# Kernel optimization log

Hardware: AMD Instinct MI355X
Metric: run time of the kernel (lower is better)

Reference implementation:

```python
import jax, jax.numpy as jnp
import numpy as np

VOCAB = 32000
D_MODEL = 1024
D_FF = 4 * D_MODEL
N_LAYERS = 2
N_EXPERTS = 8
TOP_K = 2
BATCH = 4
SEQ = 2048
LN_EPS = 1e-5


def setup_inputs() -> dict:
    key = jax.random.key(0)
    ks = jax.random.split(key, 12)
    s = lambda *dims: 1.0 / np.sqrt(dims[-2] if len(dims) > 1 else dims[-1])
    inp = {
        "tokens": jax.random.randint(ks[0], (BATCH, SEQ), 0, VOCAB, dtype=jnp.int32),
        "symbolic_emb": jax.random.normal(ks[1], (BATCH, D_MODEL), dtype=jnp.float32),
        "emb": jax.random.normal(ks[2], (VOCAB, D_MODEL), dtype=jnp.float32) * 0.02,
        "gate_w": jax.random.normal(ks[3], (N_LAYERS, D_MODEL, N_EXPERTS), dtype=jnp.float32) / np.sqrt(D_MODEL),
        "gate_b": jnp.zeros((N_LAYERS, N_EXPERTS), dtype=jnp.float32),
        "w1": jax.random.normal(ks[4], (N_LAYERS, N_EXPERTS, D_MODEL, D_FF), dtype=jnp.float32) / np.sqrt(D_MODEL),
        "b1": jnp.zeros((N_LAYERS, N_EXPERTS, D_FF), dtype=jnp.float32),
        "w2": jax.random.normal(ks[5], (N_LAYERS, N_EXPERTS, D_FF, D_MODEL), dtype=jnp.float32) / np.sqrt(D_FF),
        "b2": jnp.zeros((N_LAYERS, N_EXPERTS, D_MODEL), dtype=jnp.float32),
        "ln_g": jnp.ones((D_MODEL,), dtype=jnp.float32),
        "ln_b": jnp.zeros((D_MODEL,), dtype=jnp.float32),
    }
    return inp


def _moe_layer(x_flat, gw, gb, w1, b1, w2, b2):
    # x_flat: [T, d]
    probs = jax.nn.softmax(x_flat @ gw + gb, axis=-1)            # [T, E]
    weights, idx = jax.lax.top_k(probs, TOP_K)                   # [T, K]
    # combine weight per (token, expert): sum of top-k weights routed to that expert
    combine = jnp.sum(jax.nn.one_hot(idx, N_EXPERTS, dtype=x_flat.dtype) * weights[..., None], axis=1)  # [T, E]
    out = jnp.zeros_like(x_flat)
    for j in range(N_EXPERTS):  # small fixed structural loop
        h = jax.nn.gelu(x_flat @ w1[j] + b1[j], approximate=False)  # [T, d_ff]
        y = h @ w2[j] + b2[j]                                       # [T, d]
        out = out + combine[:, j:j + 1] * y
    return out


def reference(tokens, symbolic_emb, emb, gate_w, gate_b, w1, b1, w2, b2, ln_g, ln_b):
    x = emb[tokens] + symbolic_emb[:, None, :]                  # [B, S, d]
    T = BATCH * SEQ
    x = x.reshape(T, D_MODEL)
    for l in range(N_LAYERS):
        x = _moe_layer(x, gate_w[l], gate_b[l], w1[l], b1[l], w2[l], b2[l])
    mu = jnp.mean(x, axis=-1, keepdims=True)
    var = jnp.mean(jnp.square(x - mu), axis=-1, keepdims=True)
    x = (x - mu) * jax.lax.rsqrt(var + LN_EPS) * ln_g + ln_b
    return x.reshape(BATCH, SEQ, D_MODEL)
```

## Files before the change

### kernel.cpp

```cpp
#include <hip/hip_runtime.h>
#include <math.h>

#define T_TOK 8192
#define DM 1024
#define DFF 4096
#define NE 8
#define NPAIR 16384
#define MT256 72
#define MT128 136
#define LN_EPS 1e-5f

typedef __attribute__((ext_vector_type(8))) short bf16x8;
typedef __attribute__((ext_vector_type(4))) float f32x4;
typedef __attribute__((ext_vector_type(4))) unsigned short u16x4;
typedef __attribute__((ext_vector_type(8))) unsigned short u16x8;
typedef unsigned int u32;
typedef unsigned short u16;

__device__ __forceinline__ u16 f2bf(float f) {
  union { float f; u32 u; } v; v.f = f;
  u32 r = (v.u + 0x7fffu + ((v.u >> 16) & 1u)) >> 16;
  return (u16)r;
}
__device__ __forceinline__ float bf2f(u16 h) {
  union { u32 u; float f; } v; v.u = ((u32)h) << 16; return v.f;
}
__device__ __forceinline__ float gelu_exact(float v) {
  return 0.5f * v * (1.0f + erff(v * 0.70710678118654752f));
}
__device__ __forceinline__ float gelu_fast(float v) {
  float u = v * (0.7978845608f + 0.0356774081f * v * v);
  float t = __expf(-2.0f * fabsf(u));
  float th = (1.0f - t) / (1.0f + t);
  th = copysignf(th, u);
  return 0.5f * v * (1.0f + th);
}

__device__ __forceinline__ void gll16(const void* g, void* l) {
  __builtin_amdgcn_global_load_lds(
      (const __attribute__((address_space(1))) u32*)g,
      (__attribute__((address_space(3))) u32*)l, 16, 0, 0);
}

__device__ __forceinline__ void xcd_remap(int& M, int& nt) {
  if (((gridDim.x & 7) == 0) && ((gridDim.y & 7) == 0)) {
    int c = blockIdx.x & 7, q = blockIdx.x >> 3;
    M  = ((blockIdx.y >> 3) << 3) + c;
    nt = (q << 3) + (blockIdx.y & 7);
  } else {
    M = blockIdx.y; nt = blockIdx.x;
  }
}

__global__ __launch_bounds__(256) void embed_gate_kernel(const int* __restrict__ tok,
    const float* __restrict__ sym, const float* __restrict__ emb,
    const float* __restrict__ gw, const float* __restrict__ gb,
    u16* __restrict__ xh, u16* __restrict__ xl,
    int* __restrict__ topk_idx, float* __restrict__ topk_w)
{
  int t = blockIdx.x;
  int b = t >> 11;
  int tk = tok[t];
  int d = threadIdx.x * 4;
  f32x4 e = *(const f32x4*)(emb + (size_t)tk * DM + d);
  f32x4 s = *(const f32x4*)(sym + (size_t)b * DM + d);
  f32x4 v = e + s;
  u16x4 hv, lv;
#pragma unroll
  for (int j = 0; j < 4; ++j) {
    u16 hb = f2bf(v[j]);
    hv[j] = hb;
    lv[j] = f2bf(v[j] - bf2f(hb));
  }
  *(u16x4*)(xh + (size_t)t * DM + d) = hv;
  *(u16x4*)(xl + (size_t)t * DM + d) = lv;

  double a[8] = {0,0,0,0,0,0,0,0};
#pragma unroll
  for (int q = 0; q < 4; ++q) {
    const f32x4* gr = (const f32x4*)(gw + (size_t)(d + q) * 8);
    f32x4 g0 = gr[0], g1 = gr[1];
    double xv = (double)v[q];
    a[0] += xv*(double)g0.x; a[1] += xv*(double)g0.y;
    a[2] += xv*(double)g0.z; a[3] += xv*(double)g0.w;
    a[4] += xv*(double)g1.x; a[5] += xv*(double)g1.y;
    a[6] += xv*(double)g1.z; a[7] += xv*(double)g1.w;
  }
#pragma unroll
  for (int j = 0; j < 8; ++j) {
#pragma unroll
    for (int sh = 32; sh; sh >>= 1) a[j] += __shfl_xor(a[j], sh);
  }
  __shared__ double red[4][8];
  int wave = threadIdx.x >> 6, lane = threadIdx.x & 63;
  if (lane == 0) {
#pragma unroll
    for (int j = 0; j < 8; ++j) red[wave][j] = a[j];
  }
  __syncthreads();
  if (threadIdx.x == 0) {
    double lg[8];
#pragma unroll
    for (int j = 0; j < 8; ++j)
      lg[j] = red[0][j] + red[1][j] + red[2][j] + red[3][j] + (double)gb[j];
    double m = lg[0];
    for (int j = 1; j < 8; ++j) m = lg[j] > m ? lg[j] : m;
    double p[8], sum = 0.0;
    for (int j = 0; j < 8; ++j) { p[j] = exp(lg[j] - m); sum += p[j]; }
    for (int j = 0; j < 8; ++j) p[j] /= sum;
    int j0 = 0; double b0 = p[0];
    for (int j = 1; j < 8; ++j) if (p[j] > b0) { b0 = p[j]; j0 = j; }
    int j1 = (j0 == 0) ? 1 : 0; double b1v = p[j1];
    for (int j = 0; j < 8; ++j) if (j != j0 && p[j] > b1v) { b1v = p[j]; j1 = j; }
    topk_idx[t*2]   = j0; topk_idx[t*2+1] = j1;
    topk_w[t*2]     = (float)b0; topk_w[t*2+1] = (float)b1v;
  }
}

__global__ __launch_bounds__(256) void count_kernel(const int* __restrict__ topk_idx,
    int* __restrict__ meta)
{
  __shared__ int hist[8];
  int tid = threadIdx.x;
  if (tid < 8) hist[tid] = 0;
  __syncthreads();
  int t = blockIdx.x * 256 + tid;
  atomicAdd(&hist[topk_idx[t*2] & 7], 1);
  atomicAdd(&hist[topk_idx[t*2+1] & 7], 1);
  __syncthreads();
  if (tid < 8) meta[256 + blockIdx.x * 8 + tid] = hist[tid];
}

__global__ __launch_bounds__(64) void scan_kernel(int* __restrict__ meta)
{
  __shared__ int tot[8], off[9], tb2[8], tb1[8];
  int lane = threadIdx.x;
  if (lane < 8) {
    int s = 0;
    for (int b = 0; b < 32; ++b) s += meta[256 + b * 8 + lane];
    tot[lane] = s;
  }
  __syncthreads();
  if (lane == 0) {
    int s = 0, n2 = 0, n1 = 0;
    for (int e = 0; e < 8; ++e) {
      off[e] = s; s += tot[e];
      tb2[e] = n2; n2 += (tot[e] + 255) >> 8;
      tb1[e] = n1; n1 += (tot[e] + 127) >> 7;
    }
    off[8] = s;
    for (int i = n2; i < MT256; ++i) meta[32 + i] = -1;
    for (int i = n1; i < MT128; ++i) meta[104 + i] = -1;
  }
  __syncthreads();
  if (lane < 9) meta[8 + lane] = off[lane];
  if (lane < 8) {
    meta[lane] = tot[lane];
    int n2 = (tot[lane] + 255) >> 8;
    for (int i = 0; i < n2; ++i) meta[32 + tb2[lane] + i] = (lane << 16) | i;
    int n1 = (tot[lane] + 127) >> 7;
    for (int i = 0; i < n1; ++i) meta[104 + tb1[lane] + i] = (lane << 16) | i;
    int run = off[lane];
    for (int b = 0; b < 32; ++b) {
      meta[512 + b * 8 + lane] = run;
      run += meta[256 + b * 8 + lane];
    }
  }
}

__global__ __launch_bounds__(256) void scatter_kernel(int* __restrict__ topk_idx,
    const int* __restrict__ meta, int* __restrict__ pair_token)
{
  __shared__ int hist[8];
  __shared__ int base[8];
  int tid = threadIdx.x;
  if (tid < 8) { hist[tid] = 0; base[tid] = meta[512 + blockIdx.x * 8 + tid]; }
  __syncthreads();
  int t = blockIdx.x * 256 + tid;
#pragma unroll
  for (int k = 0; k < 2; ++k) {
    int e = topk_idx[t*2 + k] & 7;
    int pos = atomicAdd(&hist[e], 1);
    int slot = base[e] + pos;
    pair_token[slot] = t;
    topk_idx[t*2 + k] = e | (slot << 3);
  }
}

template<bool LO>
__global__ __launch_bounds__(256) void transpose_kernel(const float* __restrict__ src,
    u16* __restrict__ dsth, u16* __restrict__ dstl, int K, int N)
{
  __shared__ float tile[64][65];
  int e = blockIdx.z;
  const float* s = src + (size_t)e * K * N;
  size_t dbase = (size_t)e * K * N;
  int n0 = blockIdx.x * 64, k0 = blockIdx.y * 64;
  int tid = threadIdx.x;
#pragma unroll
  for (int j = 0; j < 4; ++j) {
    int kl = j * 16 + (tid >> 4);
    int nn = (tid & 15) * 4;
    f32x4 v = *(const f32x4*)(s + (size_t)(k0 + kl) * N + n0 + nn);
    tile[nn + 0][kl] = v.x;
    tile[nn + 1][kl] = v.y;
    tile[nn + 2][kl] = v.z;
    tile[nn + 3][kl] = v.w;
  }
  __syncthreads();
#pragma unroll
  for (int it = 0; it < 2; ++it) {
    int task = it * 256 + tid;
    int nr = task >> 3;
    int ch = task & 7;
    u16x8 oh, ol;
#pragma unroll
    for (int j = 0; j < 8; ++j) {
      float v = tile[nr][ch*8 + j];
      u16 hb = f2bf(v);
      oh[j] = hb;
      if (LO) ol[j] = f2bf(v - bf2f(hb));
    }
    size_t doff = dbase + (size_t)(n0 + nr) * K + k0 + ch*8;
    *(u16x8*)(dsth + doff) = oh;
    if (LO) *(u16x8*)(dstl + doff) = ol;
  }
}

__global__ __launch_bounds__(256) void w2g_kernel(const float* __restrict__ w2,
    const float* __restrict__ gw, float* __restrict__ w2g)
{
  int wid = blockIdx.x * 4 + (threadIdx.x >> 6);
  int lane = threadIdx.x & 63;
  int e = wid >> 12, f = wid & 4095;
  const float* row = w2 + ((size_t)e * DFF + f) * DM;
  float a0=0,a1=0,a2=0,a3=0,a4=0,a5=0,a6=0,a7=0;
  for (int i = 0; i < 4; ++i) {
    int d0 = i * 256 + lane * 4;
    f32x4 xv = *(const f32x4*)(row + d0);
#pragma unroll
    for (int q = 0; q < 4; ++q) {
      const f32x4* gr = (const f32x4*)(gw + (size_t)(d0 + q) * 8);
      f32x4 g0 = gr[0], g1 = gr[1];
      float xq = xv[q];
      a0 += xq*g0.x; a1 += xq*g0.y; a2 += xq*g0.z; a3 += xq*g0.w;
      a4 += xq*g1.x; a5 += xq*g1.y; a6 += xq*g1.z; a7 += xq*g1.w;
    }
  }
  float acc[8] = {a0,a1,a2,a3,a4,a5,a6,a7};
#pragma unroll
  for (int j = 0; j < 8; ++j) {
#pragma unroll
    for (int sh = 32; sh; sh >>= 1) acc[j] += __shfl_xor(acc[j], sh);
  }
  if (lane == 0) {
#pragma unroll
    for (int j = 0; j < 8; ++j) w2g[(size_t)wid * 8 + j] = acc[j];
  }
}

__global__ __launch_bounds__(256) void b2g_kernel(const float* __restrict__ b2,
    const float* __restrict__ gw, float* __restrict__ b2g)
{
  int w = blockIdx.x * 4 + (threadIdx.x >> 6);
  int lane = threadIdx.x & 63;
  int e = w >> 3, j = w & 7;
  float acc = 0.f;
  for (int i = 0; i < 16; ++i) {
    int d = i * 64 + lane;
    acc += b2[(size_t)e * DM + d] * gw[(size_t)d * 8 + j];
  }
#pragma unroll
  for (int sh = 32; sh; sh >>= 1) acc += __shfl_xor(acc, sh);
  if (lane == 0) b2g[w] = acc;
}

__global__ __launch_bounds__(256) void gate1_kernel(const float* __restrict__ Rpart,
    const float* __restrict__ b2g, const float* __restrict__ gb,
    int* __restrict__ topk_idx, float* __restrict__ topk_w)
{
  int t = blockIdx.x * 256 + threadIdx.x;
  int v0 = topk_idx[t*2], v1 = topk_idx[t*2+1];
  int e0 = v0 & 7, e1 = v1 & 7;
  int s0 = v0 >> 3, s1 = v1 >> 3;
  float r0[8] = {0,0,0,0,0,0,0,0}, r1[8] = {0,0,0,0,0,0,0,0};
  for (int nt = 0; nt < 16; ++nt) {
    const float* p0r = Rpart + ((size_t)nt * NPAIR + s0) * 8;
    const float* p1r = Rpart + ((size_t)nt * NPAIR + s1) * 8;
#pragma unroll
    for (int j = 0; j < 8; ++j) { r0[j] += p0r[j]; r1[j] += p1r[j]; }
  }
  double w0 = (double)topk_w[t*2], w1 = (double)topk_w[t*2+1];
  double a[8];
#pragma unroll
  for (int j = 0; j < 8; ++j)
    a[j] = w0 * ((double)r0[j] + (double)b2g[e0*8+j])
         + w1 * ((double)r1[j] + (double)b2g[e1*8+j])
         + (double)gb[j];
  double m = a[0];
  for (int j = 1; j < 8; ++j) m = a[j] > m ? a[j] : m;
  double p[8], sum = 0.0;
  for (int j = 0; j < 8; ++j) { p[j] = exp(a[j] - m); sum += p[j]; }
  for (int j = 0; j < 8; ++j) p[j] /= sum;
  int j0 = 0; double b0 = p[0];
  for (int j = 1; j < 8; ++j) if (p[j] > b0) { b0 = p[j]; j0 = j; }
  int j1 = (j0 == 0) ? 1 : 0; double b1v = p[j1];
  for (int j = 0; j < 8; ++j) if (j != j0 && p[j] > b1v) { b1v = p[j]; j1 = j; }
  topk_idx[t*2]   = j0; topk_idx[t*2+1] = j1;
  topk_w[t*2]     = (float)b0; topk_w[t*2+1] = (float)b1v;
}

template<int K0, int NSEG, int NTOT, bool GATHER>
__global__ __launch_bounds__(512, 2) void gemm256_kernel(
    const u16* __restrict__ Ah, const u16* __restrict__ Al,
    const u16* __restrict__ Bh, const u16* __restrict__ Bl,
    const float* __restrict__ bias, const int* __restrict__ off,
    const int* __restrict__ tiletab, const int* __restrict__ pair_token,
    u16* __restrict__ outh, const float* __restrict__ W2G,
    float* __restrict__ Rpart)
{
  constexpr int NT = (K0 * NSEG) / 64;
  static_assert(NT >= 2 && (NT & 1) == 0, "");
  int Mi, nti;
  xcd_remap(Mi, nti);
  const int tt = tiletab[Mi];
  if (tt < 0) return;
  const int e  = tt >> 16;
  const int mt = tt & 0xffff;
  const int off_e = off[e], off_e1 = off[e + 1];
  const int p0 = off_e + mt * 256;
  const int n0 = nti * 256;

  __shared__ __align__(16) u16 ALs[2][2][8192];
  __shared__ __align__(16) u16 BLs[2][2][8192];

  const int tid  = threadIdx.x;
  const int lane = tid & 63;
  const int wave = tid >> 6;
  const int wm = wave >> 2;
  const int wn = wave & 3;
  const int wbase = tid & 448;

  size_t aoff[2], boff[2];
#pragma unroll
  for (int i = 0; i < 2; ++i) {
    int c = i * 512 + tid;
    int r = c >> 2;
    int cs = (c & 3) ^ ((r >> 1) & 3);
    int idx = p0 + r;
    if (idx >= off_e1) idx = p0;
    int ar = GATHER ? pair_token[idx] : idx;
    aoff[i] = (size_t)ar * K0 + (size_t)(cs * 8);
    boff[i] = ((size_t)e * NTOT + n0 + r) * K0 + (size_t)(cs * 8);
  }

  auto stageA = [&](int t, int kh) {
    int kk = t * 64 + kh * 32;
    int seg = (NSEG == 3) ? (kk >> 10) : 0;
    int kc  = (NSEG == 3) ? (kk & (K0 - 1)) : kk;
    const u16* base = (NSEG == 3 && seg == 1) ? Al : Ah;
    u16* dst = &ALs[t & 1][kh][0];
#pragma unroll
    for (int i = 0; i < 2; ++i)
      gll16(base + aoff[i] + kc, dst + (i * 512 + wbase) * 8);
  };
  auto stageB = [&](int t, int kh) {
    int kk = t * 64 + kh * 32;
    int seg = (NSEG == 3) ? (kk >> 10) : 0;
    int kc  = (NSEG == 3) ? (kk & (K0 - 1)) : kk;
    const u16* base = (NSEG == 3 && seg == 2) ? Bl : Bh;
    u16* dst = &BLs[t & 1][kh][0];
#pragma unroll
    for (int i = 0; i < 2; ++i)
      gll16(base + boff[i] + kc, dst + (i * 512 + wbase) * 8);
  };

  f32x4 acc[8][4];
  const f32x4 fzero = {0.f, 0.f, 0.f, 0.f};
#pragma unroll
  for (int m = 0; m < 8; ++m)
#pragma unroll
    for (int n = 0; n < 4; ++n) acc[m][n] = fzero;

  const int swzB = (((lane >> 4) ^ (((lane & 15) >> 1) & 3)) << 4);
  const char* Abase = (const char*)&ALs[0][0][0]
      + (wm * 128 + (lane & 15)) * 64 + swzB;
  const char* Bbase = (const char*)&BLs[0][0][0]
      + (wn * 64 + (lane & 15)) * 64 + swzB;

#define RDA4(dst, POFS, MB)                                                     \
  { _Pragma("unroll") for (int mf = 0; mf < 4; ++mf)                            \
      dst[mf] = *(const bf16x8*)(Abase + (POFS) + ((MB) + mf) * 1024); }
#define RDB4(dst, POFS)                                                         \
  { _Pragma("unroll") for (int nf = 0; nf < 4; ++nf)                            \
      dst[nf] = *(const bf16x8*)(Bbase + (POFS) + nf * 1024); }

#define MMBLK(MB, A4, B4)                                                       \
  {                                                                             \
    __builtin_amdgcn_s_setprio(1);                                              \
    _Pragma("unroll")                                                           \
    for (int mf = 0; mf < 4; ++mf)                                              \
      _Pragma("unroll")                                                         \
      for (int nf = 0; nf < 4; ++nf)                                            \
        acc[(MB) + mf][nf] = __builtin_amdgcn_mfma_f32_16x16x32_bf16(           \
            (A4)[mf], (B4)[nf], acc[(MB) + mf][nf], 0, 0, 0);                   \
    __builtin_amdgcn_s_setprio(0);                                              \
  }

#define TILE256(t, POFS)                                                        \
  {                                                                             \
    bf16x8 bA[4], aA[4], aB[4], bC[4], aC[4], aD[4];                            \
    RDB4(bA, (POFS));                                                           \
    RDA4(aA, (POFS), 0);                                                        \
    if ((t) + 1 < NT) stageA((t) + 1, 1);                                       \
    __builtin_amdgcn_s_barrier();                                               \
    MMBLK(0, aA, bA);                                                           \
    __builtin_amdgcn_s_barrier();                                               \
    RDA4(aB, (POFS), 4);                                                        \
    if ((t) + 1 < NT) stageB((t) + 1, 1);                                       \
    __builtin_amdgcn_s_barrier();                                               \
    MMBLK(4, aB, bA);                                                           \
    if ((t) + 1 < NT) { asm volatile("s_waitcnt vmcnt(8)" ::: "memory"); }      \
    else              { asm volatile("s_waitcnt vmcnt(0)" ::: "memory"); }      \
    __builtin_amdgcn_s_barrier();                                               \
    asm volatile("" ::: "memory");                                              \
    RDB4(bC, (POFS) + 16384);                                                   \
    RDA4(aC, (POFS) + 16384, 0);                                                \
    if ((t) + 2 < NT) stageA((t) + 2, 0);                                       \
    __builtin_amdgcn_s_barrier();                                               \
    MMBLK(0, aC, bC);                                                           \
    __builtin_amdgcn_s_barrier();                                               \
    RDA4(aD, (POFS) + 16384, 4);                                                \
    if ((t) + 2 < NT) stageB((t) + 2, 0);                                       \
    __builtin_amdgcn_s_barrier();                                               \
    MMBLK(4, aD, bC);                                                           \
    if ((t) + 1 < NT) {                                                         \
      if ((t) + 2 < NT) { asm volatile("s_waitcnt vmcnt(8)" ::: "memory"); }    \
      else              { asm volatile("s_waitcnt vmcnt(4)" ::: "memory"); }    \
      __builtin_amdgcn_s_barrier();                                             \
      asm volatile("" ::: "memory");                                            \
    }                                                                           \
  }

  stageA(0, 0); stageB(0, 0);
  stageA(0, 1); stageB(0, 1);
  stageA(1, 0); stageB(1, 0);
  asm volatile("s_waitcnt vmcnt(8)" ::: "memory");
  __builtin_amdgcn_s_barrier();
  asm volatile("" ::: "memory");

  for (int t = 0; t < NT; t += 2) {
    TILE256(t, 0);
    TILE256(t + 1, 32768);
  }
#undef TILE256
#undef MMBLK
#undef RDA4
#undef RDB4

  float bv[4];
#pragma unroll
  for (int nf = 0; nf < 4; ++nf)
    bv[nf] = bias[(size_t)e * NTOT + n0 + wn * 64 + nf * 16 + (lane & 15)];

  __syncthreads();
  float* Rpt = (float*)&ALs[0][0][0];
  f32x4 wg0[4], wg1[4];
#pragma unroll
  for (int nf = 0; nf < 4; ++nf) {
    int col = n0 + wn * 64 + nf * 16 + (lane & 15);
    const float* wp = W2G + ((size_t)e * NTOT + col) * 8;
    wg0[nf] = *(const f32x4*)wp;
    wg1[nf] = *(const f32x4*)(wp + 4);
  }
#pragma unroll
  for (int mf = 0; mf < 8; ++mf) {
    f32x4 pr0[4], pr1[4];
#pragma unroll
    for (int r = 0; r < 4; ++r) { pr0[r] = fzero; pr1[r] = fzero; }
    int rbase = p0 + wm * 128 + mf * 16 + ((lane >> 4) << 2);
#pragma unroll
    for (int nf = 0; nf < 4; ++nf) {
      int col = n0 + wn * 64 + nf * 16 + (lane & 15);
#pragma unroll
      for (int r = 0; r < 4; ++r) {
        float v = gelu_exact(acc[mf][nf][r] + bv[nf]);
        if (rbase + r < off_e1)
          outh[(size_t)(rbase + r) * NTOT + col] = f2bf(v);
        pr0[r] += v * wg0[nf];
        pr1[r] += v * wg1[nf];
      }
    }
#pragma unroll
    for (int r = 0; r < 4; ++r) {
#pragma unroll
      for (int sh = 1; sh < 16; sh <<= 1) {
#pragma unroll
        for (int q = 0; q < 4; ++q) {
          pr0[r][q] += __shfl_xor(pr0[r][q], sh);
          pr1[r][q] += __shfl_xor(pr1[r][q], sh);
        }
      }
      if ((lane & 15) == 0) {
        int rl = wm * 128 + mf * 16 + ((lane >> 4) << 2) + r;
        float* dst = Rpt + ((size_t)(wn * 256 + rl)) * 8;
        *(f32x4*)dst = pr0[r];
        *(f32x4*)(dst + 4) = pr1[r];
      }
    }
  }
  __syncthreads();
  for (int i = tid; i < 256 * 8; i += 512) {
    int rl = i >> 3, j = i & 7;
    float ssum = Rpt[(size_t)(0 * 256 + rl) * 8 + j]
               + Rpt[(size_t)(1 * 256 + rl) * 8 + j]
               + Rpt[(size_t)(2 * 256 + rl) * 8 + j]
               + Rpt[(size_t)(3 * 256 + rl) * 8 + j];
    int p = p0 + rl;
    if (p < off_e1)
      Rpart[((size_t)nti * NPAIR + p) * 8 + j] = ssum;
  }
}

template<int K0, int NTOT, bool GATHER, int MODE>
__global__ __launch_bounds__(256, 4) void gemm128_kernel(
    const u16* __restrict__ Ah, const u16* __restrict__ Bh,
    const float* __restrict__ bias, const int* __restrict__ off,
    const int* __restrict__ tiletab, const int* __restrict__ pair_token,
    u16* __restrict__ outp)
{
  constexpr int NT = K0 / 32;
  static_assert((NT & 1) == 0, "");
  int Mi, nti;
  xcd_remap(Mi, nti);
  const int tt = tiletab[Mi];
  if (tt < 0) return;
  const int e  = tt >> 16;
  const int mt = tt & 0xffff;
  const int off_e = off[e], off_e1 = off[e + 1];
  const int p0 = off_e + mt * 128;
  const int n0 = nti * 128;

  __shared__ __align__(16) u16 AL[2][4096];
  __shared__ __align__(16) u16 BL[2][4096];

  const int tid  = threadIdx.x;
  const int lane = tid & 63;
  const int wave = tid >> 6;
  const int wm = wave >> 1, wn = wave & 1;
  const int wbase = tid & 192;

  size_t aoff[2], boff[2];
#pragma unroll
  for (int i = 0; i < 2; ++i) {
    int c = i * 256 + tid;
    int r = c >> 2;
    int cs = (c & 3) ^ ((r >> 1) & 3);
    int idx = p0 + r;
    if (idx >= off_e1) idx = p0;
    int ar = GATHER ? pair_token[idx] : idx;
    aoff[i] = (size_t)ar * K0 + (size_t)(cs * 8);
    boff[i] = ((size_t)e * NTOT + n0 + r) * K0 + (size_t)(cs * 8);
  }

  auto stage = [&](int b, int t) {
    int kc = t * 32;
#pragma unroll
    for (int i = 0; i < 2; ++i) {
      int cb = i * 256 + wbase;
      gll16(Ah + aoff[i] + kc, &AL[b][cb * 8]);
      gll16(Bh + boff[i] + kc, &BL[b][cb * 8]);
    }
  };

  f32x4 acc[4][4];
  const f32x4 fzero = {0.f, 0.f, 0.f, 0.f};
#pragma unroll
  for (int m = 0; m < 4; ++m)
#pragma unroll
    for (int n = 0; n < 4; ++n) acc[m][n] = fzero;

  const int swzB = (((lane >> 4) ^ (((lane & 15) >> 1) & 3)) << 4);
  const char* Abase = (const char*)&AL[0][0]
      + (wm * 64 + (lane & 15)) * 64 + swzB;
  const char* Bbase = (const char*)&BL[0][0]
      + (wn * 64 + (lane & 15)) * 64 + swzB;

#define MMA128(BOFS)                                                            \
  {                                                                             \
    bf16x8 af[4], bf[4];                                                        \
    _Pragma("unroll")                                                           \
    for (int m = 0; m < 4; ++m)                                                 \
      af[m] = *(const bf16x8*)(Abase + (BOFS) + m * 1024);                      \
    _Pragma("unroll")                                                           \
    for (int n = 0; n < 4; ++n)                                                 \
      bf[n] = *(const bf16x8*)(Bbase + (BOFS) + n * 1024);                      \
    __builtin_amdgcn_s_setprio(1);                                              \
    _Pragma("unroll")                                                           \
    for (int m = 0; m < 4; ++m)                                                 \
      _Pragma("unroll")                                                         \
      for (int n = 0; n < 4; ++n)                                               \
        acc[m][n] = __builtin_amdgcn_mfma_f32_16x16x32_bf16(                    \
            af[m], bf[n], acc[m][n], 0, 0, 0);                                  \
    __builtin_amdgcn_s_setprio(0);                                              \
  }

  stage(0, 0);
  __syncthreads();

  for (int t = 0; t < NT; t += 2) {
    stage(1, t + 1);
    MMA128(0);
    __syncthreads();
    if (t + 2 < NT) stage(0, t + 2);
    MMA128(8192);
    __syncthreads();
  }
#undef MMA128

  float bv[4];
#pragma unroll
  for (int n = 0; n < 4; ++n)
    bv[n] = bias[(size_t)e * NTOT + n0 + wn * 64 + n * 16 + (lane & 15)];

#pragma unroll
  for (int m = 0; m < 4; ++m) {
    int rbase = p0 + wm * 64 + m * 16 + ((lane >> 4) << 2);
#pragma unroll
    for (int n = 0; n < 4; ++n) {
      int col = n0 + wn * 64 + n * 16 + (lane & 15);
#pragma unroll
      for (int r = 0; r < 4; ++r) {
        int rowp = rbase + r;
        if (rowp < off_e1) {
          float v = acc[m][n][r] + bv[n];
          if constexpr (MODE == 0) v = gelu_fast(v);
          outp[(size_t)rowp * NTOT + col] = f2bf(v);
        }
      }
    }
  }
}

__global__ __launch_bounds__(256) void combine0_kernel(const u16* __restrict__ yb,
    const int* __restrict__ topk_idx, const float* __restrict__ topk_w,
    u16* __restrict__ xh)
{
  int t = blockIdx.x;
  int d = threadIdx.x * 4;
  int s0 = topk_idx[t*2] >> 3, s1 = topk_idx[t*2 + 1] >> 3;
  float w0 = topk_w[t*2], w1 = topk_w[t*2 + 1];
  u16x4 y0 = *(const u16x4*)(yb + (size_t)s0 * DM + d);
  u16x4 y1 = *(const u16x4*)(yb + (size_t)s1 * DM + d);
  u16x4 hv;
#pragma unroll
  for (int j = 0; j < 4; ++j)
    hv[j] = f2bf(bf2f(y0[j]) * w0 + bf2f(y1[j]) * w1);
  *(u16x4*)(xh + (size_t)t * DM + d) = hv;
}

__global__ __launch_bounds__(256) void combine1_ln_kernel(const u16* __restrict__ yb,
    const int* __restrict__ topk_idx, const float* __restrict__ topk_w,
    const float* __restrict__ g, const float* __restrict__ b, float* __restrict__ out)
{
  int t = blockIdx.x;
  int d = threadIdx.x * 4;
  int s0 = topk_idx[t*2] >> 3, s1 = topk_idx[t*2 + 1] >> 3;
  float w0 = topk_w[t*2], w1 = topk_w[t*2 + 1];
  u16x4 y0 = *(const u16x4*)(yb + (size_t)s0 * DM + d);
  u16x4 y1 = *(const u16x4*)(yb + (size_t)s1 * DM + d);
  f32x4 v;
#pragma unroll
  for (int j = 0; j < 4; ++j)
    v[j] = bf2f(y0[j]) * w0 + bf2f(y1[j]) * w1;
  float s = v.x + v.y + v.z + v.w;
  float sq = v.x*v.x + v.y*v.y + v.z*v.z + v.w*v.w;
#pragma unroll
  for (int sh = 32; sh; sh >>= 1) { s += __shfl_xor(s, sh); sq += __shfl_xor(sq, sh); }
  __shared__ float red[8];
  int wave = threadIdx.x >> 6, lane = threadIdx.x & 63;
  if (lane == 0) { red[wave] = s; red[4 + wave] = sq; }
  __syncthreads();
  s = red[0] + red[1] + red[2] + red[3];
  sq = red[4] + red[5] + red[6] + red[7];
  float mu = s * (1.0f / DM);
  float var = sq * (1.0f / DM) - mu * mu;
  float inv = rsqrtf(var + LN_EPS);
  f32x4 gv = *(const f32x4*)(g + d);
  f32x4 bv = *(const f32x4*)(b + d);
  f32x4 o;
  o.x = (v.x - mu) * inv * gv.x + bv.x;
  o.y = (v.y - mu) * inv * gv.y + bv.y;
  o.z = (v.z - mu) * inv * gv.z + bv.z;
  o.w = (v.w - mu) * inv * gv.w + bv.w;
  *(f32x4*)(out + (size_t)t * DM + d) = o;
}

extern "C" void kernel_launch(void* const* d_in, const int* in_sizes, int n_in,
                              void* d_out, int out_size, void* d_ws, size_t ws_size,
                              hipStream_t stream)
{
  const int*   tokens = (const int*)d_in[0];
  const float* sym    = (const float*)d_in[1];
  const float* emb    = (const float*)d_in[2];
  const float* gate_w = (const float*)d_in[3];
  const float* gate_b = (const float*)d_in[4];
  const float* w1     = (const float*)d_in[5];
  const float* b1     = (const float*)d_in[6];
  const float* w2     = (const float*)d_in[7];
  const float* b2     = (const float*)d_in[8];
  const float* ln_g   = (const float*)d_in[9];
  const float* ln_b   = (const float*)d_in[10];

  char* ws = (char*)d_ws;
  u16*   yb  = (u16*)  (ws);
  u16*   xh  = (u16*)  (ws + 33554432);
  u16*   xl  = (u16*)  (ws + 50331648);
  u16*   hh  = (u16*)  (ws + 67108864);
  float* W2G   = (float*)(ws + 201326592);
  float* Rpart = (float*)(ws + 202375168);
  float* B2G   = (float*)(ws + 219152384);
  u16*   wTh = (u16*)  (ws + 335544320);
  u16*   wTl = (u16*)  (ws + 402653184);
  int*   pair_token = (int*)  (ws + 469762048);
  int*   topk_idx   = (int*)  (ws + 469893120);
  float* topk_w     = (float*)(ws + 469958656);
  int*   meta       = (int*)  (ws + 470024192);

  embed_gate_kernel<<<T_TOK, 256, 0, stream>>>(tokens, sym, emb, gate_w, gate_b,
                                               xh, xl, topk_idx, topk_w);
  count_kernel<<<T_TOK / 256, 256, 0, stream>>>(topk_idx, meta);
  scan_kernel<<<1, 64, 0, stream>>>(meta);
  scatter_kernel<<<T_TOK / 256, 256, 0, stream>>>(topk_idx, meta, pair_token);

  w2g_kernel<<<NE * DFF / 4, 256, 0, stream>>>(w2, gate_w + (size_t)DM * NE, W2G);
  b2g_kernel<<<16, 256, 0, stream>>>(b2, gate_w + (size_t)DM * NE, B2G);

  transpose_kernel<true><<<dim3(DFF / 64, DM / 64, NE), 256, 0, stream>>>(
      w1, wTh, wTl, DM, DFF);
  gemm256_kernel<DM, 3, DFF, true><<<dim3(DFF / 256, MT256), 512, 0, stream>>>(
      xh, xl, wTh, wTl, b1, meta + 8, meta + 32, pair_token, hh, W2G, Rpart);

  transpose_kernel<false><<<dim3(DM / 64, DFF / 64, NE), 256, 0, stream>>>(
      w2, wTh, nullptr, DFF, DM);
  gemm128_kernel<DFF, DM, false, 2><<<dim3(DM / 128, MT128), 256, 0, stream>>>(
      hh, wTh, b2, meta + 8, meta + 104, pair_token, yb);

  combine0_kernel<<<T_TOK, 256, 0, stream>>>(yb, topk_idx, topk_w, xh);

  gate1_kernel<<<T_TOK / 256, 256, 0, stream>>>(Rpart, B2G, gate_b + NE,
                                                topk_idx, topk_w);
  count_kernel<<<T_TOK / 256, 256, 0, stream>>>(topk_idx, meta);
  scan_kernel<<<1, 64, 0, stream>>>(meta);
  scatter_kernel<<<T_TOK / 256, 256, 0, stream>>>(topk_idx, meta, pair_token);

  transpose_kernel<false><<<dim3(DFF / 64, DM / 64, NE), 256, 0, stream>>>(
      w1 + (size_t)NE * DM * DFF, wTh, nullptr, DM, DFF);
  gemm128_kernel<DM, DFF, true, 0><<<dim3(DFF / 128, MT128), 256, 0, stream>>>(
      xh, wTh, b1 + (size_t)NE * DFF, meta + 8, meta + 104, pair_token, hh);

  transpose_kernel<false><<<dim3(DM / 64, DFF / 64, NE), 256, 0, stream>>>(
      w2 + (size_t)NE * DFF * DM, wTh, nullptr, DFF, DM);
  gemm128_kernel<DFF, DM, false, 2><<<dim3(DM / 128, MT128), 256, 0, stream>>>(
      hh, wTh, b2 + (size_t)NE * DM, meta + 8, meta + 104, pair_token, yb);

  combine1_ln_kernel<<<T_TOK, 256, 0, stream>>>(yb, topk_idx, topk_w,
                                                ln_g, ln_b, (float*)d_out);
}
```

Baseline: 1.500 ms.

## Triple-buffer LDS in gemm128 with prefetch distance two and vmcnt waits

Moves the 128x128 grouped GEMM from a double-buffered shared-memory pipeline to a triple-buffered one. Each k-step now prefetches the tile two steps ahead and waits only for the loads of the next tile, using a partial s_waitcnt vmcnt before a raw barrier, instead of a full __syncthreads. The aim is to hide more global-load latency behind the MFMA work. In exchange, LDS use grows to 48KB per block and the occupancy hint drops from 4 to 3 blocks per CU. The loop is unrolled by three with a fixed two-step tail, which requires NT%3==2.

```diff
diff --git a/kernel.cpp b/kernel.cpp
--- a/kernel.cpp
+++ b/kernel.cpp
@@ -523,14 +523,14 @@
 }
 
 template<int K0, int NTOT, bool GATHER, int MODE>
-__global__ __launch_bounds__(256, 4) void gemm128_kernel(
+__global__ __launch_bounds__(256, 3) void gemm128_kernel(
     const u16* __restrict__ Ah, const u16* __restrict__ Bh,
     const float* __restrict__ bias, const int* __restrict__ off,
     const int* __restrict__ tiletab, const int* __restrict__ pair_token,
     u16* __restrict__ outp)
 {
   constexpr int NT = K0 / 32;
-  static_assert((NT & 1) == 0, "");
+  static_assert(NT % 3 == 2 && NT >= 5, "tail layout assumes NT%3==2");
   int Mi, nti;
   xcd_remap(Mi, nti);
   const int tt = tiletab[Mi];
@@ -541,8 +541,8 @@
   const int p0 = off_e + mt * 128;
   const int n0 = nti * 128;
 
-  __shared__ __align__(16) u16 AL[2][4096];
-  __shared__ __align__(16) u16 BL[2][4096];
+  __shared__ __align__(16) u16 AL[3][4096];
+  __shared__ __align__(16) u16 BL[3][4096];
 
   const int tid  = threadIdx.x;
   const int lane = tid & 63;
@@ -563,13 +563,15 @@
     boff[i] = ((size_t)e * NTOT + n0 + r) * K0 + (size_t)(cs * 8);
   }
 
-  auto stage = [&](int b, int t) {
+  auto stage_ofs = [&](int sofs, int t) {
     int kc = t * 32;
+    u16* a = (u16*)((char*)&AL[0][0] + sofs);
+    u16* b = (u16*)((char*)&BL[0][0] + sofs);
 #pragma unroll
     for (int i = 0; i < 2; ++i) {
       int cb = i * 256 + wbase;
-      gll16(Ah + aoff[i] + kc, &AL[b][cb * 8]);
-      gll16(Bh + boff[i] + kc, &BL[b][cb * 8]);
+      gll16(Ah + aoff[i] + kc, a + cb * 8);
+      gll16(Bh + boff[i] + kc, b + cb * 8);
     }
   };
 
@@ -586,15 +588,16 @@
   const char* Bbase = (const char*)&BL[0][0]
       + (wn * 64 + (lane & 15)) * 64 + swzB;
 
-#define MMA128(BOFS)                                                            \
+#define G128STEP(T, CUR, PRE)                                                   \
   {                                                                             \
+    if ((T) + 2 < NT) stage_ofs((PRE), (T) + 2);                                \
     bf16x8 af[4], bf[4];                                                        \
     _Pragma("unroll")                                                           \
     for (int m = 0; m < 4; ++m)                                                 \
-      af[m] = *(const bf16x8*)(Abase + (BOFS) + m * 1024);                      \
+      af[m] = *(const bf16x8*)(Abase + (CUR) + m * 1024);                       \
     _Pragma("unroll")                                                           \
     for (int n = 0; n < 4; ++n)                                                 \
-      bf[n] = *(const bf16x8*)(Bbase + (BOFS) + n * 1024);                      \
+      bf[n] = *(const bf16x8*)(Bbase + (CUR) + n * 1024);                       \
     __builtin_amdgcn_s_setprio(1);                                              \
     _Pragma("unroll")                                                           \
     for (int m = 0; m < 4; ++m)                                                 \
@@ -603,20 +606,28 @@
         acc[m][n] = __builtin_amdgcn_mfma_f32_16x16x32_bf16(                    \
             af[m], bf[n], acc[m][n], 0, 0, 0);                                  \
     __builtin_amdgcn_s_setprio(0);                                              \
-  }
-
-  stage(0, 0);
-  __syncthreads();
-
-  for (int t = 0; t < NT; t += 2) {
-    stage(1, t + 1);
-    MMA128(0);
-    __syncthreads();
-    if (t + 2 < NT) stage(0, t + 2);
-    MMA128(8192);
-    __syncthreads();
-  }
-#undef MMA128
+    if ((T) + 1 < NT) {                                                         \
+      if ((T) + 2 < NT) { asm volatile("s_waitcnt vmcnt(4)" ::: "memory"); }    \
+      else              { asm volatile("s_waitcnt vmcnt(0)" ::: "memory"); }    \
+      __builtin_amdgcn_s_barrier();                                             \
+      asm volatile("" ::: "memory");                                            \
+    }                                                                           \
+  }
+
+  stage_ofs(0, 0);
+  stage_ofs(8192, 1);
+  asm volatile("s_waitcnt vmcnt(4)" ::: "memory");
+  __builtin_amdgcn_s_barrier();
+  asm volatile("" ::: "memory");
+
+  for (int t3 = 0; t3 + 3 <= NT; t3 += 3) {
+    G128STEP(t3 + 0, 0,     16384);
+    G128STEP(t3 + 1, 8192,  0);
+    G128STEP(t3 + 2, 16384, 8192);
+  }
+  G128STEP(NT - 2, 0,    16384);
+  G128STEP(NT - 1, 8192, 0);
+#undef G128STEP
 
   float bv[4];
 #pragma unroll
```

Result: no change. 1.501 ms (+0.1%).
